# Kernel tuning notes

Hardware: AMD Instinct MI355X
Metric: run time of the kernel (lower is better)

Reference implementation:

```python
import jax, jax.numpy as jnp
import numpy as np

KSIZE = 7
SIGMA = 3.0
ALPHA = 0.1
POS_VAL_FOR_ALL_NEG = 5.0
NEG_VAL_FOR_ALL_POS = -5.0


def _gauss_kernel():
    x = jnp.arange(KSIZE, dtype=jnp.float32) - (KSIZE - 1) / 2.0
    pdf = jnp.exp(-0.5 * (x / SIGMA) ** 2)
    return pdf / pdf.sum()


def _gaussian_blur(img):
    # img: (B, C, H, W); separable 7x7 gaussian, reflect padding (torchvision behavior)
    B, C, H, W = img.shape
    k = _gauss_kernel()
    pad = KSIZE // 2
    x = jnp.pad(img, ((0, 0), (0, 0), (pad, pad), (pad, pad)), mode='reflect')
    x = x.reshape(B * C, 1, H + 2 * pad, W + 2 * pad)
    kh = k.reshape(1, 1, KSIZE, 1)
    kw = k.reshape(1, 1, 1, KSIZE)
    x = jax.lax.conv_general_dilated(x, kh, (1, 1), 'VALID')
    x = jax.lax.conv_general_dilated(x, kw, (1, 1), 'VALID')
    return x.reshape(B, C, H, W)


def _dup_map(x, mask, fallback):
    # x, mask: (L,). Gather x[mask] (original order) then tile to length L.
    # Stable argsort puts True(=selected) positions first in original order.
    L = x.shape[0]
    cnt = mask.sum()
    order = jnp.argsort(jnp.logical_not(mask))  # selected indices first, stable
    idx = order[jnp.arange(L) % jnp.maximum(cnt, 1)]
    return jnp.where(cnt == 0, jnp.float32(fallback), x[idx])


_dup_vmapped = jax.vmap(_dup_map, in_axes=(0, 0, None))


def _bce_with_logits(x, y):
    # mean( max(x,0) - x*y + log1p(exp(-|x|)) ) == mean( softplus(x) - x*y )
    return jnp.mean(jnp.logaddexp(0.0, x) - x * y)


def _forward(inp, tgt):
    B, C, H, W = inp.shape
    aug_sim_target = (_gaussian_blur(tgt * 255.0) > 0).astype(jnp.float32)

    L = H * W
    x = inp.reshape(B * C, L)
    t = tgt.reshape(B * C, L)
    a = aug_sim_target.reshape(B * C, L)

    # duplicated_pos: gather input at target>0, tile; fallback +5 if no positives
    pos_mask = t > 0
    dup_pos = _dup_vmapped(x, pos_mask, POS_VAL_FOR_ALL_NEG)

    # duplicated_false_pos: prefer (input>0 & ~aug_pos); else all negatives; else -5
    aug_pos = a > 0
    fp_mask = jnp.logical_and(x > 0, jnp.logical_not(aug_pos))
    neg_mask = jnp.logical_not(aug_pos)
    cnt_fp = fp_mask.sum(axis=1, keepdims=True)
    chosen_mask = jnp.where(cnt_fp > 0, fp_mask, neg_mask)
    dup_fp = _dup_vmapped(x, chosen_mask, NEG_VAL_FOR_ALL_POS)

    sim = dup_pos * x
    aug_sim = dup_pos * dup_fp

    sim_loss = _bce_with_logits(sim, t) + _bce_with_logits(dup_pos, jnp.ones_like(x))
    aug_sim_loss = _bce_with_logits(aug_sim, jnp.zeros_like(x))
    return sim_loss + ALPHA * aug_sim_loss


def setup_inputs() -> dict:
    key = jax.random.key(0)
    k1, k2 = jax.random.split(key)
    B, C, H, W = 16, 3, 512, 512
    inp = jax.random.normal(k1, (B, C, H, W), dtype=jnp.float32)
    tgt = jax.random.randint(k2, (B, C, H, W), 0, 2).astype(jnp.float32)
    return {"input": inp, "target": tgt}


def reference(input, target):
    return _forward(input, target)
```

## Files before the change

### kernel.cpp

```cpp
#include <hip/hip_runtime.h>
#include <math.h>

constexpr int W = 512;
constexpr int HIMG = 512;
constexpr int L = 1 << 18;
constexpr int LOG2L = 18;
constexpr int TPB = 256;
constexpr int TILE = 2048;
constexpr int TILES_PER_ROW = L / TILE;
constexpr int WORDS_PER_TILE = TILE / 64;
constexpr int SPB = 32;
constexpr int HALO = 3;
constexpr int HBUF = SPB + 2 * HALO;
constexpr int BLK_PER_IMG = HIMG / SPB;
constexpr int LBLK = 32;
constexpr int CHUNK = L / LBLK;
constexpr int LIT = CHUNK / (TPB * 4);

typedef unsigned long long ull;

__device__ __forceinline__ float softplus_f(float v) {
    return fmaxf(v, 0.0f) +
           0.6931471805599453f *
               __builtin_amdgcn_logf(1.0f + __builtin_amdgcn_exp2f(-fabsf(v) * 1.4426950408889634f));
}

__device__ __forceinline__ ull hdil7(ull prev, ull cur, ull next) {
    ull r = cur;
    r |= (cur >> 1) | (next << 63);
    r |= (cur >> 2) | (next << 62);
    r |= (cur >> 3) | (next << 61);
    r |= (cur << 1) | (prev >> 63);
    r |= (cur << 2) | (prev >> 62);
    r |= (cur << 3) | (prev >> 61);
    return r;
}

template <typename T>
__device__ __forceinline__ T sel8(const T* a, int k) {
    return k == 0 ? a[0] : k == 1 ? a[1] : k == 2 ? a[2] : k == 3 ? a[3]
         : k == 4 ? a[4] : k == 5 ? a[5] : k == 6 ? a[6] : a[7];
}

__global__ __launch_bounds__(TPB)
void fused_mask_kernel(const float* __restrict__ x, const float* __restrict__ t,
                       ull* __restrict__ mT, ull* __restrict__ mFp, ull* __restrict__ mNeg,
                       int* __restrict__ cPos, int* __restrict__ cFp, int* __restrict__ cNeg,
                       float* __restrict__ out) {
    if (blockIdx.x == 0 && threadIdx.x == 0) out[0] = 0.0f;
    int b = blockIdx.x;
    int img = b >> 4;
    int y0 = (b & 15) * SPB;
    int gs0 = img * HIMG + y0;

    __shared__ ull hbuf[HBUF][8];
    __shared__ ull tbuf[SPB][8];
    __shared__ ull xbuf[SPB][8];

    int lane = threadIdx.x & 63;
    int wv = threadIdx.x >> 6;
    int ylo = (y0 - HALO < 0) ? 0 : y0 - HALO;
    int yhi = (y0 + SPB - 1 + HALO > HIMG - 1) ? HIMG - 1 : y0 + SPB - 1 + HALO;

    for (int yl = ylo + wv; yl <= yhi; yl += 4) {
        int gbase = (img * HIMG + yl) * W;
        bool own = (yl >= y0) && (yl < y0 + SPB);
        ull wt[8], wx[8], h[8];
#pragma unroll
        for (int k = 0; k < 8; ++k) wt[k] = __ballot(t[gbase + k * 64 + lane] > 0.0f);
        if (own) {
#pragma unroll
            for (int k = 0; k < 8; ++k) wx[k] = __ballot(x[gbase + k * 64 + lane] > 0.0f);
        }
#pragma unroll
        for (int k = 0; k < 8; ++k) {
            ull cur = wt[k];
            ull prev = k ? wt[k - 1]
                         : ((((cur >> 1) & 1ull) << 63) | (((cur >> 2) & 1ull) << 62) |
                            (((cur >> 3) & 1ull) << 61));
            ull next = (k < 7) ? wt[k + 1]
                               : (((cur >> 62) & 1ull) | (((cur >> 61) & 1ull) << 1) |
                                  (((cur >> 60) & 1ull) << 2));
            h[k] = hdil7(prev, cur, next);
        }
        int hy = yl - (y0 - HALO);
        int k = lane & 7;
        if (lane < 8) {
            hbuf[hy][k] = sel8(h, k);
        } else if (own && lane < 16) {
            tbuf[yl - y0][k] = sel8(wt, k);
            mT[(img * HIMG + yl) * 8 + k] = sel8(wt, k);
        } else if (own && lane < 24) {
            xbuf[yl - y0][k] = sel8(wx, k);
        }
    }
    __syncthreads();

    int tid = threadIdx.x;
    int ys = tid >> 3;
    int c = tid & 7;
    int y = y0 + ys;
    ull wa = 0;
#pragma unroll
    for (int d = -3; d <= 3; ++d) {
        int yy = y + d;
        yy = yy < 0 ? -yy : (yy > HIMG - 1 ? 2 * (HIMG - 1) - yy : yy);
        wa |= hbuf[yy - (y0 - HALO)][c];
    }
    ull tw = tbuf[ys][c];
    ull fp = xbuf[ys][c] & ~wa;
    ull ng = ~wa;
    int gw = gs0 * 8 + tid;
    mFp[gw] = fp;
    mNeg[gw] = ng;
    int pT = __popcll(tw), pF = __popcll(fp), pN = __popcll(ng);
#pragma unroll
    for (int m = 1; m < 32; m <<= 1) {
        pT += __shfl_xor(pT, m, 64);
        pF += __shfl_xor(pF, m, 64);
        pN += __shfl_xor(pN, m, 64);
    }
    if ((lane & 31) == 0) {
        int tile = img * TILES_PER_ROW + (y0 >> 2) + (tid >> 5);
        cPos[tile] = pT; cFp[tile] = pF; cNeg[tile] = pN;
    }
}

__global__ void scan_kernel(const int* __restrict__ cPos, const int* __restrict__ cFp,
                            const int* __restrict__ cNeg,
                            int* __restrict__ oPos, int* __restrict__ oCh,
                            int* __restrict__ rCp, int* __restrict__ rCc,
                            ull* __restrict__ rMp, ull* __restrict__ rMc,
                            int* __restrict__ rUseFp) {
    int r = blockIdx.x;
    int tid = threadIdx.x;
    __shared__ int ssp[TILES_PER_ROW], ssf[TILES_PER_ROW], ssn[TILES_PER_ROW];
    int myp = cPos[r * TILES_PER_ROW + tid];
    int myf = cFp[r * TILES_PER_ROW + tid];
    int myn = cNeg[r * TILES_PER_ROW + tid];
    ssp[tid] = myp; ssf[tid] = myf; ssn[tid] = myn;
    __syncthreads();
    for (int off = 1; off < TILES_PER_ROW; off <<= 1) {
        int ap = 0, af = 0, an = 0;
        if (tid >= off) { ap = ssp[tid - off]; af = ssf[tid - off]; an = ssn[tid - off]; }
        __syncthreads();
        if (tid >= off) { ssp[tid] += ap; ssf[tid] += af; ssn[tid] += an; }
        __syncthreads();
    }
    int cp = ssp[TILES_PER_ROW - 1], cf = ssf[TILES_PER_ROW - 1], cn = ssn[TILES_PER_ROW - 1];
    bool useFp = cf > 0;
    int tile = r * TILES_PER_ROW + tid;
    oPos[tile] = ssp[tid] - myp;
    oCh[tile] = useFp ? (ssf[tid] - myf) : (ssn[tid] - myn);
    if (tid == 0) {
        int cc = useFp ? cf : cn;
        rCp[r] = cp; rCc[r] = cc; rUseFp[r] = useFp ? 1 : 0;
        ull dp_ = (ull)(cp > 0 ? cp : 1);
        ull dc_ = (ull)(cc > 0 ? cc : 1);
        rMp[r] = ((1ull << 40) + dp_ - 1) / dp_;
        rMc[r] = ((1ull << 40) + dc_ - 1) / dc_;
    }
}

__global__ __launch_bounds__(TPB)
void scatter_kernel(const float* __restrict__ x, const ull* __restrict__ mT,
                    const ull* __restrict__ mFp, const ull* __restrict__ mNeg,
                    const int* __restrict__ oPos, const int* __restrict__ oCh,
                    const int* __restrict__ rUseFp,
                    float* __restrict__ xp, float* __restrict__ xf) {
    int tile = blockIdx.x;
    int tid = threadIdx.x;
    int r = tile >> 7;
    bool useFp = rUseFp[r] != 0;
    int widx = tile * WORDS_PER_TILE + (tid >> 3);
    int shift = (tid & 7) * 8;
    unsigned bT = (unsigned)(mT[widx] >> shift) & 0xFF;
    ull chw = useFp ? mFp[widx] : mNeg[widx];
    unsigned bCh = (unsigned)(chw >> shift) & 0xFF;
    const float4* x4 = (const float4*)x;
    int b4 = tile * (TILE / 4) + tid * 2;
    float4 a = x4[b4], b = x4[b4 + 1];
    float xv[8] = {a.x, a.y, a.z, a.w, b.x, b.y, b.z, b.w};
    int p = __popc(bT), c = __popc(bCh);
    __shared__ int s[TPB];
    __shared__ float bufP[TILE], bufC[TILE];
    int v = p | (c << 16);
    s[tid] = v;
    __syncthreads();
    for (int off = 1; off < TPB; off <<= 1) {
        int add = tid >= off ? s[tid - off] : 0;
        __syncthreads();
        s[tid] += add;
        __syncthreads();
    }
    int excl = s[tid] - v;
    int ep = excl & 0xFFFF;
    int ec = excl >> 16;
#pragma unroll
    for (int e = 0; e < 8; ++e) {
        if ((bT >> e) & 1) bufP[ep++] = xv[e];
        if ((bCh >> e) & 1) bufC[ec++] = xv[e];
    }
    __syncthreads();
    int tot = s[TPB - 1];
    int P = tot & 0xFFFF, C = tot >> 16;
    int rL = r << LOG2L;
    int pbase = rL + oPos[tile];
    for (int i = tid; i < P; i += TPB) xp[pbase + i] = bufP[i];
    int cbase = rL + oCh[tile];
    for (int i = tid; i < C; i += TPB) xf[cbase + i] = bufC[i];
}

__global__ __launch_bounds__(TPB)
void loss_kernel(const float* __restrict__ x, const ull* __restrict__ mT,
                 const float* __restrict__ xp, const float* __restrict__ xf,
                 const int* __restrict__ rCp, const int* __restrict__ rCc,
                 const ull* __restrict__ rMp, const ull* __restrict__ rMc,
                 float* __restrict__ out, double inv_ntot) {
    int r = blockIdx.x >> 5;
    int cb = (blockIdx.x & 31) * CHUNK;
    int rL = r << LOG2L;
    int cp = rCp[r], cc = rCc[r];
    ull Mp = rMp[r], Mc = rMc[r];
    const float4* x4 = (const float4*)(x + rL + cb);
    const float* xpr = xp + rL;
    const float* xfr = xf + rL;
    const ull* mtr = mT + (rL >> 6);
    float local = 0.0f;
#pragma unroll
    for (int it = 0; it < LIT; ++it) {
        int o4 = it * TPB + threadIdx.x;
        unsigned l = (unsigned)(cb + (o4 << 2));
        float4 xv = x4[o4];
        unsigned tb = (unsigned)(mtr[l >> 6] >> (l & 63)) & 0xFu;
        float dps[4], dfs[4];
        if (cp > 0) {
            unsigned d = (unsigned)cp;
            unsigned q = (unsigned)(((ull)l * Mp) >> 40);
            unsigned m0 = l - q * d;
            unsigned m1 = m0 + 1; if (m1 == d) m1 = 0;
            unsigned m2 = m1 + 1; if (m2 == d) m2 = 0;
            unsigned m3 = m2 + 1; if (m3 == d) m3 = 0;
            dps[0] = xpr[m0]; dps[1] = xpr[m1]; dps[2] = xpr[m2]; dps[3] = xpr[m3];
        } else {
            dps[0] = dps[1] = dps[2] = dps[3] = 5.0f;
        }
        if (cc > 0) {
            unsigned d = (unsigned)cc;
            unsigned q = (unsigned)(((ull)l * Mc) >> 40);
            unsigned m0 = l - q * d;
            unsigned m1 = m0 + 1; if (m1 == d) m1 = 0;
            unsigned m2 = m1 + 1; if (m2 == d) m2 = 0;
            unsigned m3 = m2 + 1; if (m3 == d) m3 = 0;
            dfs[0] = xfr[m0]; dfs[1] = xfr[m1]; dfs[2] = xfr[m2]; dfs[3] = xfr[m3];
        } else {
            dfs[0] = dfs[1] = dfs[2] = dfs[3] = -5.0f;
        }
        float xs[4] = {xv.x, xv.y, xv.z, xv.w};
#pragma unroll
        for (int k = 0; k < 4; ++k) {
            float sim = dps[k] * xs[k];
            float e = softplus_f(sim) + softplus_f(-dps[k]) + 0.1f * softplus_f(dps[k] * dfs[k]);
            if ((tb >> k) & 1) e -= sim;
            local += e;
        }
    }
    __shared__ double sd[TPB];
    int tid = threadIdx.x;
    sd[tid] = (double)local;
    __syncthreads();
    for (int off = TPB / 2; off > 0; off >>= 1) {
        if (tid < off) sd[tid] += sd[tid + off];
        __syncthreads();
    }
    if (tid == 0) atomicAdd(out, (float)(sd[0] * inv_ntot));
}

extern "C" void kernel_launch(void* const* d_in, const int* in_sizes, int n_in,
                              void* d_out, int out_size, void* d_ws, size_t ws_size,
                              hipStream_t stream) {
    const float* x = (const float*)d_in[0];
    const float* t = (const float*)d_in[1];
    float* out = (float*)d_out;

    int ntot = in_sizes[0];
    int R = ntot >> LOG2L;
    int numTiles = ntot / TILE;
    int nwords = ntot / 64;
    int nMaskBlk = ntot / (SPB * W);

    char* ws = (char*)d_ws;
    size_t off = 0;
    auto alloc = [&](size_t bytes) {
        size_t p = off;
        off = (off + bytes + 255) & ~(size_t)255;
        return (void*)(ws + p);
    };
    ull* mT   = (ull*)alloc((size_t)nwords * 8);
    ull* mFp  = (ull*)alloc((size_t)nwords * 8);
    ull* mNeg = (ull*)alloc((size_t)nwords * 8);
    int* cPos = (int*)alloc(numTiles * sizeof(int));
    int* cFp  = (int*)alloc(numTiles * sizeof(int));
    int* cNeg = (int*)alloc(numTiles * sizeof(int));
    int* oPos = (int*)alloc(numTiles * sizeof(int));
    int* oCh  = (int*)alloc(numTiles * sizeof(int));
    int* rCp = (int*)alloc(R * sizeof(int));
    int* rCc = (int*)alloc(R * sizeof(int));
    int* rUseFp = (int*)alloc(R * sizeof(int));
    ull* rMp = (ull*)alloc(R * sizeof(ull));
    ull* rMc = (ull*)alloc(R * sizeof(ull));
    float* xp = (float*)alloc((size_t)ntot * sizeof(float));
    float* xf = (float*)alloc((size_t)ntot * sizeof(float));

    fused_mask_kernel<<<nMaskBlk, TPB, 0, stream>>>(x, t, mT, mFp, mNeg, cPos, cFp, cNeg, out);
    scan_kernel<<<R, TILES_PER_ROW, 0, stream>>>(cPos, cFp, cNeg, oPos, oCh,
                                                 rCp, rCc, rMp, rMc, rUseFp);
    scatter_kernel<<<numTiles, TPB, 0, stream>>>(x, mT, mFp, mNeg, oPos, oCh, rUseFp, xp, xf);
    loss_kernel<<<R * LBLK, TPB, 0, stream>>>(x, mT, xp, xf, rCp, rCc, rMp, rMc, out,
                                              1.0 / (double)ntot);
}
```

Before: 171.0 us.

## Batch loads ahead of compute and remap loss grid across XCDs

The loss kernel now issues all x, target-bit and duplicated-positive gathers for a thread's iterations before computing, so more memory requests are in flight at once. It also doubles the number of blocks per row (halving each block's work) and permutes the block index so consecutive logical chunks spread across the eight XCDs. The risks are higher register pressure from the hoisted arrays, and more atomic adds from the larger grid.

```diff
diff --git a/kernel.cpp b/kernel.cpp
--- a/kernel.cpp
+++ b/kernel.cpp
@@ -13,7 +13,8 @@
 constexpr int HALO = 3;
 constexpr int HBUF = SPB + 2 * HALO;
 constexpr int BLK_PER_IMG = HIMG / SPB;
-constexpr int LBLK = 32;
+constexpr int LBLK = 64;
+constexpr int LOG2LBLK = 6;
 constexpr int CHUNK = L / LBLK;
 constexpr int LIT = CHUNK / (TPB * 4);
 
@@ -217,8 +218,10 @@
                  const int* __restrict__ rCp, const int* __restrict__ rCc,
                  const ull* __restrict__ rMp, const ull* __restrict__ rMc,
                  float* __restrict__ out, double inv_ntot) {
-    int r = blockIdx.x >> 5;
-    int cb = (blockIdx.x & 31) * CHUNK;
+    int nper = (int)gridDim.x >> 3;
+    int logical = ((int)blockIdx.x >> 3) + ((int)blockIdx.x & 7) * nper;
+    int r = logical >> LOG2LBLK;
+    int cb = (logical & (LBLK - 1)) * CHUNK;
     int rL = r << LOG2L;
     int cp = rCp[r], cc = rCc[r];
     ull Mp = rMp[r], Mc = rMc[r];
@@ -226,47 +229,65 @@
     const float* xpr = xp + rL;
     const float* xfr = xf + rL;
     const ull* mtr = mT + (rL >> 6);
-    float local = 0.0f;
+    int tid = threadIdx.x;
+
+    float4 xv[LIT];
+    unsigned tb[LIT];
+    float dps[LIT][4];
+#pragma unroll
+    for (int it = 0; it < LIT; ++it) xv[it] = x4[it * TPB + tid];
 #pragma unroll
     for (int it = 0; it < LIT; ++it) {
-        int o4 = it * TPB + threadIdx.x;
-        unsigned l = (unsigned)(cb + (o4 << 2));
-        float4 xv = x4[o4];
-        unsigned tb = (unsigned)(mtr[l >> 6] >> (l & 63)) & 0xFu;
-        float dps[4], dfs[4];
-        if (cp > 0) {
-            unsigned d = (unsigned)cp;
+        unsigned l = (unsigned)(cb + ((it * TPB + tid) << 2));
+        tb[it] = (unsigned)(mtr[l >> 6] >> (l & 63)) & 0xFu;
+    }
+    if (cp > 0) {
+        unsigned d = (unsigned)cp;
+#pragma unroll
+        for (int it = 0; it < LIT; ++it) {
+            unsigned l = (unsigned)(cb + ((it * TPB + tid) << 2));
             unsigned q = (unsigned)(((ull)l * Mp) >> 40);
             unsigned m0 = l - q * d;
             unsigned m1 = m0 + 1; if (m1 == d) m1 = 0;
             unsigned m2 = m1 + 1; if (m2 == d) m2 = 0;
             unsigned m3 = m2 + 1; if (m3 == d) m3 = 0;
-            dps[0] = xpr[m0]; dps[1] = xpr[m1]; dps[2] = xpr[m2]; dps[3] = xpr[m3];
-        } else {
-            dps[0] = dps[1] = dps[2] = dps[3] = 5.0f;
-        }
-        if (cc > 0) {
-            unsigned d = (unsigned)cc;
+            dps[it][0] = xpr[m0]; dps[it][1] = xpr[m1];
+            dps[it][2] = xpr[m2]; dps[it][3] = xpr[m3];
+        }
+    } else {
+#pragma unroll
+        for (int it = 0; it < LIT; ++it)
+            dps[it][0] = dps[it][1] = dps[it][2] = dps[it][3] = 5.0f;
+    }
+
+    float local = 0.0f;
+    bool hasC = cc > 0;
+    unsigned dC = (unsigned)(hasC ? cc : 1);
+#pragma unroll
+    for (int it = 0; it < LIT; ++it) {
+        float dfs[4];
+        if (hasC) {
+            unsigned l = (unsigned)(cb + ((it * TPB + tid) << 2));
             unsigned q = (unsigned)(((ull)l * Mc) >> 40);
-            unsigned m0 = l - q * d;
-            unsigned m1 = m0 + 1; if (m1 == d) m1 = 0;
-            unsigned m2 = m1 + 1; if (m2 == d) m2 = 0;
-            unsigned m3 = m2 + 1; if (m3 == d) m3 = 0;
+            unsigned m0 = l - q * dC;
+            unsigned m1 = m0 + 1; if (m1 == dC) m1 = 0;
+            unsigned m2 = m1 + 1; if (m2 == dC) m2 = 0;
+            unsigned m3 = m2 + 1; if (m3 == dC) m3 = 0;
             dfs[0] = xfr[m0]; dfs[1] = xfr[m1]; dfs[2] = xfr[m2]; dfs[3] = xfr[m3];
         } else {
             dfs[0] = dfs[1] = dfs[2] = dfs[3] = -5.0f;
         }
-        float xs[4] = {xv.x, xv.y, xv.z, xv.w};
+        float xs[4] = {xv[it].x, xv[it].y, xv[it].z, xv[it].w};
 #pragma unroll
         for (int k = 0; k < 4; ++k) {
-            float sim = dps[k] * xs[k];
-            float e = softplus_f(sim) + softplus_f(-dps[k]) + 0.1f * softplus_f(dps[k] * dfs[k]);
-            if ((tb >> k) & 1) e -= sim;
+            float dp = dps[it][k];
+            float sim = dp * xs[k];
+            float e = softplus_f(sim) + softplus_f(-dp) + 0.1f * softplus_f(dp * dfs[k]);
+            if ((tb[it] >> k) & 1) e -= sim;
             local += e;
         }
     }
     __shared__ double sd[TPB];
-    int tid = threadIdx.x;
     sd[tid] = (double)local;
     __syncthreads();
     for (int off = TPB / 2; off > 0; off >>= 1) {
```

After: 190.5 us. 1.11x slower.

## Use wave-shuffle scans and software-pipelined gathers in scatter and loss kernels

Applied to the files above, without the earlier changes.

The scatter kernel's shared-memory block scan, which needed many barriers, is replaced by a 64-lane shuffle scan plus a small cross-wave combine. The loss kernel doubles its block count, double-buffers the next iteration's x, mask and gathered loads ahead of the compute, and makes the gathers branchless via clamped divisors. Its final reduction becomes shuffle-based. The double buffering raises register pressure, which the added launch-bounds occupancy hint must contain, and the larger grid doubles the number of atomic adds to the output.

```diff
diff --git a/kernel.cpp b/kernel.cpp
--- a/kernel.cpp
+++ b/kernel.cpp
@@ -13,7 +13,8 @@
 constexpr int HALO = 3;
 constexpr int HBUF = SPB + 2 * HALO;
 constexpr int BLK_PER_IMG = HIMG / SPB;
-constexpr int LBLK = 32;
+constexpr int LBLK = 64;
+constexpr int LOG2LBLK = 6;
 constexpr int CHUNK = L / LBLK;
 constexpr int LIT = CHUNK / (TPB * 4);
 
@@ -170,6 +171,8 @@
                     float* __restrict__ xp, float* __restrict__ xf) {
     int tile = blockIdx.x;
     int tid = threadIdx.x;
+    int lane = tid & 63;
+    int wv = tid >> 6;
     int r = tile >> 7;
     bool useFp = rUseFp[r] != 0;
     int widx = tile * WORDS_PER_TILE + (tid >> 3);
@@ -182,28 +185,32 @@
     float4 a = x4[b4], b = x4[b4 + 1];
     float xv[8] = {a.x, a.y, a.z, a.w, b.x, b.y, b.z, b.w};
     int p = __popc(bT), c = __popc(bCh);
-    __shared__ int s[TPB];
+    int v = p | (c << 16);
+    int incl = v;
+#pragma unroll
+    for (int off = 1; off < 64; off <<= 1) {
+        int n = __shfl_up(incl, off, 64);
+        if (lane >= off) incl += n;
+    }
+    __shared__ int wtot[4];
     __shared__ float bufP[TILE], bufC[TILE];
-    int v = p | (c << 16);
-    s[tid] = v;
-    __syncthreads();
-    for (int off = 1; off < TPB; off <<= 1) {
-        int add = tid >= off ? s[tid - off] : 0;
-        __syncthreads();
-        s[tid] += add;
-        __syncthreads();
-    }
-    int excl = s[tid] - v;
+    if (lane == 63) wtot[wv] = incl;
+    __syncthreads();
+    int base = 0;
+    if (wv > 0) base += wtot[0];
+    if (wv > 1) base += wtot[1];
+    if (wv > 2) base += wtot[2];
+    int excl = base + incl - v;
+    int tot = wtot[0] + wtot[1] + wtot[2] + wtot[3];
     int ep = excl & 0xFFFF;
-    int ec = excl >> 16;
+    int ec = (excl >> 16) & 0xFFFF;
 #pragma unroll
     for (int e = 0; e < 8; ++e) {
         if ((bT >> e) & 1) bufP[ep++] = xv[e];
         if ((bCh >> e) & 1) bufC[ec++] = xv[e];
     }
     __syncthreads();
-    int tot = s[TPB - 1];
-    int P = tot & 0xFFFF, C = tot >> 16;
+    int P = tot & 0xFFFF, C = (tot >> 16) & 0xFFFF;
     int rL = r << LOG2L;
     int pbase = rL + oPos[tile];
     for (int i = tid; i < P; i += TPB) xp[pbase + i] = bufP[i];
@@ -211,69 +218,78 @@
     for (int i = tid; i < C; i += TPB) xf[cbase + i] = bufC[i];
 }
 
-__global__ __launch_bounds__(TPB)
+#define ISSUE(IT, B)                                                                 \
+    do {                                                                             \
+        unsigned l = (unsigned)(cb + (((IT) * TPB + tid) << 2));                     \
+        xvA[B] = x4[(IT) * TPB + tid];                                               \
+        tbA[B] = (unsigned)(mtr[l >> 6] >> (l & 63)) & 0xFu;                         \
+        unsigned mp0 = l - (unsigned)(((ull)l * Mp) >> 40) * dP;                     \
+        unsigned mp1 = mp0 + 1; if (mp1 == dP) mp1 = 0;                              \
+        unsigned mp2 = mp1 + 1; if (mp2 == dP) mp2 = 0;                              \
+        unsigned mp3 = mp2 + 1; if (mp3 == dP) mp3 = 0;                              \
+        pA[B][0] = xpr[mp0]; pA[B][1] = xpr[mp1];                                    \
+        pA[B][2] = xpr[mp2]; pA[B][3] = xpr[mp3];                                    \
+        unsigned mc0 = l - (unsigned)(((ull)l * Mc) >> 40) * dC;                     \
+        unsigned mc1 = mc0 + 1; if (mc1 == dC) mc1 = 0;                              \
+        unsigned mc2 = mc1 + 1; if (mc2 == dC) mc2 = 0;                              \
+        unsigned mc3 = mc2 + 1; if (mc3 == dC) mc3 = 0;                              \
+        fA[B][0] = xfr[mc0]; fA[B][1] = xfr[mc1];                                    \
+        fA[B][2] = xfr[mc2]; fA[B][3] = xfr[mc3];                                    \
+    } while (0)
+
+__global__ __launch_bounds__(TPB, 4)
 void loss_kernel(const float* __restrict__ x, const ull* __restrict__ mT,
                  const float* __restrict__ xp, const float* __restrict__ xf,
                  const int* __restrict__ rCp, const int* __restrict__ rCc,
                  const ull* __restrict__ rMp, const ull* __restrict__ rMc,
                  float* __restrict__ out, double inv_ntot) {
-    int r = blockIdx.x >> 5;
-    int cb = (blockIdx.x & 31) * CHUNK;
+    int blk = blockIdx.x;
+    int r = blk >> LOG2LBLK;
+    int cb = (blk & (LBLK - 1)) * CHUNK;
     int rL = r << LOG2L;
     int cp = rCp[r], cc = rCc[r];
     ull Mp = rMp[r], Mc = rMc[r];
+    bool hasP = cp > 0, hasC = cc > 0;
+    unsigned dP = (unsigned)(hasP ? cp : 1);
+    unsigned dC = (unsigned)(hasC ? cc : 1);
     const float4* x4 = (const float4*)(x + rL + cb);
     const float* xpr = xp + rL;
     const float* xfr = xf + rL;
     const ull* mtr = mT + (rL >> 6);
+    int tid = threadIdx.x;
+
+    float4 xvA[2];
+    unsigned tbA[2];
+    float pA[2][4], fA[2][4];
     float local = 0.0f;
+
+    ISSUE(0, 0);
 #pragma unroll
     for (int it = 0; it < LIT; ++it) {
-        int o4 = it * TPB + threadIdx.x;
-        unsigned l = (unsigned)(cb + (o4 << 2));
-        float4 xv = x4[o4];
-        unsigned tb = (unsigned)(mtr[l >> 6] >> (l & 63)) & 0xFu;
-        float dps[4], dfs[4];
-        if (cp > 0) {
-            unsigned d = (unsigned)cp;
-            unsigned q = (unsigned)(((ull)l * Mp) >> 40);
-            unsigned m0 = l - q * d;
-            unsigned m1 = m0 + 1; if (m1 == d) m1 = 0;
-            unsigned m2 = m1 + 1; if (m2 == d) m2 = 0;
-            unsigned m3 = m2 + 1; if (m3 == d) m3 = 0;
-            dps[0] = xpr[m0]; dps[1] = xpr[m1]; dps[2] = xpr[m2]; dps[3] = xpr[m3];
-        } else {
-            dps[0] = dps[1] = dps[2] = dps[3] = 5.0f;
-        }
-        if (cc > 0) {
-            unsigned d = (unsigned)cc;
-            unsigned q = (unsigned)(((ull)l * Mc) >> 40);
-            unsigned m0 = l - q * d;
-            unsigned m1 = m0 + 1; if (m1 == d) m1 = 0;
-            unsigned m2 = m1 + 1; if (m2 == d) m2 = 0;
-            unsigned m3 = m2 + 1; if (m3 == d) m3 = 0;
-            dfs[0] = xfr[m0]; dfs[1] = xfr[m1]; dfs[2] = xfr[m2]; dfs[3] = xfr[m3];
-        } else {
-            dfs[0] = dfs[1] = dfs[2] = dfs[3] = -5.0f;
-        }
-        float xs[4] = {xv.x, xv.y, xv.z, xv.w};
+        const int cur = it & 1;
+        const int nxt = cur ^ 1;
+        if (it + 1 < LIT) ISSUE(it + 1, nxt);
+        float xs[4] = {xvA[cur].x, xvA[cur].y, xvA[cur].z, xvA[cur].w};
+        unsigned tb = tbA[cur];
 #pragma unroll
         for (int k = 0; k < 4; ++k) {
-            float sim = dps[k] * xs[k];
-            float e = softplus_f(sim) + softplus_f(-dps[k]) + 0.1f * softplus_f(dps[k] * dfs[k]);
+            float dp = hasP ? pA[cur][k] : 5.0f;
+            float df = hasC ? fA[cur][k] : -5.0f;
+            float sim = dp * xs[k];
+            float e = softplus_f(sim) + softplus_f(-dp) + 0.1f * softplus_f(dp * df);
             if ((tb >> k) & 1) e -= sim;
             local += e;
         }
     }
-    __shared__ double sd[TPB];
-    int tid = threadIdx.x;
-    sd[tid] = (double)local;
-    __syncthreads();
-    for (int off = TPB / 2; off > 0; off >>= 1) {
-        if (tid < off) sd[tid] += sd[tid + off];
-        __syncthreads();
-    }
-    if (tid == 0) atomicAdd(out, (float)(sd[0] * inv_ntot));
+
+    double v = (double)local;
+#pragma unroll
+    for (int off = 32; off > 0; off >>= 1) v += __shfl_down(v, off, 64);
+    __shared__ double wsum[4];
+    if ((tid & 63) == 0) wsum[tid >> 6] = v;
+    __syncthreads();
+    if (tid == 0)
+        atomicAdd(out, (float)((wsum[0] + wsum[1] + wsum[2] + wsum[3]) * inv_ntot));
 }
 
 extern "C" void kernel_launch(void* const* d_in, const int* in_sizes, int n_in,
```

Result: slower. 190.5 us (+11.4%).

## Stage cyclic gather windows in shared memory and use more loss blocks

Applied to the files above, without the earlier changes.

The loss kernel now preloads each block's contiguous cyclic window of the compacted positive and false-positive arrays into shared memory with coalesced loads, then reads them back as float4. This replaces four scalar per-thread gathers with modulo wraparound inside the main loop. The grid grows from 32 to 128 blocks per row and launch bounds target 8 blocks per CU. The cost is extra shared memory, a barrier, and redundant modulo work during staging. The host launch must also match the new block count.

```diff
diff --git a/kernel.cpp b/kernel.cpp
--- a/kernel.cpp
+++ b/kernel.cpp
@@ -13,9 +13,13 @@
 constexpr int HALO = 3;
 constexpr int HBUF = SPB + 2 * HALO;
 constexpr int BLK_PER_IMG = HIMG / SPB;
-constexpr int LBLK = 32;
+constexpr int LBLK = 128;
+constexpr int LOG2LBLK = 7;
 constexpr int CHUNK = L / LBLK;
 constexpr int LIT = CHUNK / (TPB * 4);
+constexpr int WIN = CHUNK + 4;
+constexpr int WSTG = WIN / TPB;
+constexpr int WREM = WIN - WSTG * TPB;
 
 typedef unsigned long long ull;
 
@@ -211,62 +215,88 @@
     for (int i = tid; i < C; i += TPB) xf[cbase + i] = bufC[i];
 }
 
-__global__ __launch_bounds__(TPB)
+__global__ __launch_bounds__(TPB, 8)
 void loss_kernel(const float* __restrict__ x, const ull* __restrict__ mT,
                  const float* __restrict__ xp, const float* __restrict__ xf,
                  const int* __restrict__ rCp, const int* __restrict__ rCc,
                  const ull* __restrict__ rMp, const ull* __restrict__ rMc,
                  float* __restrict__ out, double inv_ntot) {
-    int r = blockIdx.x >> 5;
-    int cb = (blockIdx.x & 31) * CHUNK;
+    int blk = blockIdx.x;
+    int r = blk >> LOG2LBLK;
+    int cb = (blk & (LBLK - 1)) * CHUNK;
     int rL = r << LOG2L;
     int cp = rCp[r], cc = rCc[r];
     ull Mp = rMp[r], Mc = rMc[r];
+    bool hasP = cp > 0, hasC = cc > 0;
+    unsigned dP = (unsigned)(hasP ? cp : 1);
+    unsigned dC = (unsigned)(hasC ? cc : 1);
     const float4* x4 = (const float4*)(x + rL + cb);
     const float* xpr = xp + rL;
     const float* xfr = xf + rL;
     const ull* mtr = mT + (rL >> 6);
+    int tid = threadIdx.x;
+
+    __shared__ __align__(16) float shP[WIN];
+    __shared__ __align__(16) float shF[WIN];
+
+    if (hasP) {
+        unsigned cb0 = (unsigned)cb - (unsigned)(((ull)(unsigned)cb * Mp) >> 40) * dP;
+#pragma unroll
+        for (int u = 0; u < WSTG; ++u) {
+            unsigned j = (unsigned)tid + u * TPB;
+            unsigned s = cb0 + j;
+            s -= (unsigned)(((ull)s * Mp) >> 40) * dP;
+            shP[j] = xpr[s];
+        }
+        if (tid < WREM) {
+            unsigned j = (unsigned)tid + WSTG * TPB;
+            unsigned s = cb0 + j;
+            s -= (unsigned)(((ull)s * Mp) >> 40) * dP;
+            shP[j] = xpr[s];
+        }
+    }
+    if (hasC) {
+        unsigned cb0 = (unsigned)cb - (unsigned)(((ull)(unsigned)cb * Mc) >> 40) * dC;
+#pragma unroll
+        for (int u = 0; u < WSTG; ++u) {
+            unsigned j = (unsigned)tid + u * TPB;
+            unsigned s = cb0 + j;
+            s -= (unsigned)(((ull)s * Mc) >> 40) * dC;
+            shF[j] = xfr[s];
+        }
+        if (tid < WREM) {
+            unsigned j = (unsigned)tid + WSTG * TPB;
+            unsigned s = cb0 + j;
+            s -= (unsigned)(((ull)s * Mc) >> 40) * dC;
+            shF[j] = xfr[s];
+        }
+    }
+    __syncthreads();
+
     float local = 0.0f;
 #pragma unroll
     for (int it = 0; it < LIT; ++it) {
-        int o4 = it * TPB + threadIdx.x;
+        int o4 = it * TPB + tid;
         unsigned l = (unsigned)(cb + (o4 << 2));
         float4 xv = x4[o4];
         unsigned tb = (unsigned)(mtr[l >> 6] >> (l & 63)) & 0xFu;
-        float dps[4], dfs[4];
-        if (cp > 0) {
-            unsigned d = (unsigned)cp;
-            unsigned q = (unsigned)(((ull)l * Mp) >> 40);
-            unsigned m0 = l - q * d;
-            unsigned m1 = m0 + 1; if (m1 == d) m1 = 0;
-            unsigned m2 = m1 + 1; if (m2 == d) m2 = 0;
-            unsigned m3 = m2 + 1; if (m3 == d) m3 = 0;
-            dps[0] = xpr[m0]; dps[1] = xpr[m1]; dps[2] = xpr[m2]; dps[3] = xpr[m3];
-        } else {
-            dps[0] = dps[1] = dps[2] = dps[3] = 5.0f;
-        }
-        if (cc > 0) {
-            unsigned d = (unsigned)cc;
-            unsigned q = (unsigned)(((ull)l * Mc) >> 40);
-            unsigned m0 = l - q * d;
-            unsigned m1 = m0 + 1; if (m1 == d) m1 = 0;
-            unsigned m2 = m1 + 1; if (m2 == d) m2 = 0;
-            unsigned m3 = m2 + 1; if (m3 == d) m3 = 0;
-            dfs[0] = xfr[m0]; dfs[1] = xfr[m1]; dfs[2] = xfr[m2]; dfs[3] = xfr[m3];
-        } else {
-            dfs[0] = dfs[1] = dfs[2] = dfs[3] = -5.0f;
-        }
+        float4 dp4 = *(const float4*)&shP[o4 << 2];
+        float4 df4 = *(const float4*)&shF[o4 << 2];
         float xs[4] = {xv.x, xv.y, xv.z, xv.w};
+        float dpa[4] = {dp4.x, dp4.y, dp4.z, dp4.w};
+        float dfa[4] = {df4.x, df4.y, df4.z, df4.w};
 #pragma unroll
         for (int k = 0; k < 4; ++k) {
-            float sim = dps[k] * xs[k];
-            float e = softplus_f(sim) + softplus_f(-dps[k]) + 0.1f * softplus_f(dps[k] * dfs[k]);
+            float dp = hasP ? dpa[k] : 5.0f;
+            float df = hasC ? dfa[k] : -5.0f;
+            float sim = dp * xs[k];
+            float e = softplus_f(sim) + softplus_f(-dp) + 0.1f * softplus_f(dp * df);
             if ((tb >> k) & 1) e -= sim;
             local += e;
         }
     }
+
     __shared__ double sd[TPB];
-    int tid = threadIdx.x;
     sd[tid] = (double)local;
     __syncthreads();
     for (int off = TPB / 2; off > 0; off >>= 1) {
```

New measurement: 227.8 us. 33.2% more time.
